# Kernel optimization log

Measured on AMD Instinct MI355X. Metric: run time of the kernel, lower is better.

Reference implementation:

```python
import jax, jax.numpy as jnp
import numpy as np

B, T, F, NC, H = 128, 2048, 80, 10, 32
EPS = 1e-5


def _xavier(k, shape):
    fan_out, fan_in = shape
    lim = float(np.sqrt(6.0 / (fan_in + fan_out)))
    return jax.random.uniform(k, shape, jnp.float32, -lim, lim)


def _gru_w(k, shape):
    lim = float(1.0 / np.sqrt(H))
    return jax.random.uniform(k, shape, jnp.float32, -lim, lim)


def setup_inputs() -> dict:
    key = jax.random.key(0)
    ks = jax.random.split(key, 16)
    z = jnp.zeros
    o = jnp.ones
    inp = {
        "x": jax.random.normal(ks[0], (B, T, F), jnp.float32),
        # feature extractor: Linear+BN x3
        "W1": _xavier(ks[1], (256, F)), "b1": z(256), "g1": o(256), "be1": z(256),
        "W2": _xavier(ks[2], (128, 256)), "b2": z(128), "g2": o(128), "be2": z(128),
        "W3": _xavier(ks[3], (64, 128)), "b3": z(64), "g3": o(64), "be3": z(64),
        # bidirectional GRU, hidden=32, gates ordered (r,z,n) as in torch
        "Wih_f": _gru_w(ks[4], (3 * H, 64)), "Whh_f": _gru_w(ks[5], (3 * H, H)),
        "bih_f": _gru_w(ks[6], (3 * H,)), "bhh_f": _gru_w(ks[7], (3 * H,)),
        "Wih_b": _gru_w(ks[8], (3 * H, 64)), "Whh_b": _gru_w(ks[9], (3 * H, H)),
        "bih_b": _gru_w(ks[10], (3 * H,)), "bhh_b": _gru_w(ks[11], (3 * H,)),
        # attention MLP
        "Wa1": _xavier(ks[12], (32, 64)), "ba1": z(32),
        "Wa2": _xavier(ks[13], (1, 32)), "ba2": z(1),
        # classifier
        "Wc1": _xavier(ks[14], (32, 64)), "bc1": z(32), "gc": o(32), "bec": z(32),
        "Wc2": _xavier(ks[15], (NC, 32)), "bc2": z(NC),
    }
    return inp


def _bn(x, g, b):
    # BatchNorm1d, training-mode batch statistics (biased var), dropout omitted (eval)
    m = jnp.mean(x, 0)
    v = jnp.mean(jnp.square(x - m), 0)
    return (x - m) * jax.lax.rsqrt(v + EPS) * g + b


def _gru_dir(feats, Wih, Whh, bih, bhh, reverse):
    # feats: [B,T,64] -> outputs [B,T,H]
    xp = jnp.einsum('btf,gf->btg', feats, Wih) + bih  # precompute input projections

    def step(h, xt):
        gh = h @ Whh.T + bhh
        r = jax.nn.sigmoid(xt[:, :H] + gh[:, :H])
        zg = jax.nn.sigmoid(xt[:, H:2 * H] + gh[:, H:2 * H])
        n = jnp.tanh(xt[:, 2 * H:] + r * gh[:, 2 * H:])
        hn = (1.0 - zg) * n + zg * h
        return hn, hn

    h0 = jnp.zeros((feats.shape[0], H), feats.dtype)
    _, hs = jax.lax.scan(step, h0, jnp.swapaxes(xp, 0, 1), reverse=reverse)
    return jnp.swapaxes(hs, 0, 1)


def reference(x, W1, b1, g1, be1, W2, b2, g2, be2, W3, b3, g3, be3,
              Wih_f, Whh_f, bih_f, bhh_f, Wih_b, Whh_b, bih_b, bhh_b,
              Wa1, ba1, Wa2, ba2, Wc1, bc1, gc, bec, Wc2, bc2):
    Bv, Tv, Fv = x.shape
    h = x.reshape(-1, Fv)
    h = jax.nn.relu(_bn(h @ W1.T + b1, g1, be1))
    h = jax.nn.relu(_bn(h @ W2.T + b2, g2, be2))
    h = jax.nn.relu(_bn(h @ W3.T + b3, g3, be3))
    feats = h.reshape(Bv, Tv, 64)
    gf = _gru_dir(feats, Wih_f, Whh_f, bih_f, bhh_f, False)
    gb = _gru_dir(feats, Wih_b, Whh_b, bih_b, bhh_b, True)
    gru_out = jnp.concatenate([gf, gb], axis=-1)  # [B,T,64]
    scores = jnp.tanh(gru_out @ Wa1.T + ba1) @ Wa2.T + ba2  # [B,T,1]
    attn = jax.nn.softmax(scores, axis=1)
    pooled = jnp.sum(gru_out * attn, axis=1)  # [B,64]
    c = jax.nn.relu(_bn(pooled @ Wc1.T + bc1, gc, bec))
    return c @ Wc2.T + bc2
```

## Files before the change

### kernel.cpp

```cpp
#include <hip/hip_runtime.h>
#include <hip/hip_fp16.h>
#include <cstdint>
#include <cstddef>

#define EPSV 1e-5f
constexpr int Bb = 128, Tt = 2048, Ff = 80, NCc = 10, Hh = 32;
constexpr int Nn = Bb * Tt;

constexpr size_t OFF_H1 = 0;
constexpr size_t OFF_H3 = 0;
constexpr size_t OFF_GRU = 0;
constexpr size_t OFF_XP = (size_t)Nn * 64;
constexpr size_t OFF_SCORES = (size_t)Nn * 64;
constexpr size_t OFF_H2 = (size_t)Nn * 128;
constexpr size_t TAIL = (size_t)Nn * 192;
constexpr size_t P1o = TAIL;
constexpr size_t P2o = P1o + 64 * 256 * 2;
constexpr size_t P3o = P2o + 64 * 128 * 2;
constexpr size_t PZEND = P3o + 64 * 64 * 2;
constexpr size_t SC1o = PZEND;
constexpr size_t SC2o = SC1o + 512;
constexpr size_t SC3o = SC2o + 256;
constexpr size_t BMAXo = SC3o + 128;
constexpr size_t BSUMo = BMAXo + 128;
constexpr size_t POOLEDo = BSUMo + 128;
constexpr size_t WS_EXTENT = POOLEDo + 128 * 64;

struct alignas(8) half4 { __half x, y, z, w; };

__global__ __launch_bounds__(256) void zero_kernel(float* __restrict__ p, int n) {
  const int i = blockIdx.x * 256 + threadIdx.x;
  if (i < n) p[i] = 0.f;
}

template <int K, bool BN_IN, bool STATS, bool A16, bool C16>
__global__ __launch_bounds__(256) void fc_kernel(
    const void* __restrict__ Av, const float* __restrict__ W,
    const float* __restrict__ bias, const float* __restrict__ scl,
    const float* __restrict__ shf, void* __restrict__ Cv, int ldc, int coloff,
    int COUT, float* __restrict__ Pstat) {
  __shared__ float smem[32 * 68 * 2 + 512];
  float* As = smem;
  float* Bs = smem + 32 * 68;
  float* Ss = smem + 32 * 68 * 2;
  float* Sh = Ss + 256;

  const int tid = threadIdx.x;
  const int r0 = blockIdx.x * 64;
  const int nb0 = blockIdx.y * 64;
  const int m0 = (tid >> 4) * 4;
  const int n0 = (tid & 15) * 4;

  if (BN_IN) {
    for (int k = tid; k < K; k += 256) {
      Ss[k] = scl[k];
      Sh[k] = shf[k];
    }
  }

  float acc[4][4] = {};

  constexpr int NKT = (K + 31) / 32;
  for (int kt = 0; kt < NKT; ++kt) {
    const int k0 = kt * 32;
    __syncthreads();
#pragma unroll
    for (int rep = 0; rep < 2; ++rep) {
      const int li = rep * 256 + tid;
      const int row = li >> 3;
      const int ko = (li & 7) * 4;
      float av[4] = {0.f, 0.f, 0.f, 0.f};
      if (k0 + ko < K) {
        if (A16) {
          const half4 v = *(const half4*)&(
              (const __half*)Av)[(size_t)(r0 + row) * K + k0 + ko];
          av[0] = __half2float(v.x); av[1] = __half2float(v.y);
          av[2] = __half2float(v.z); av[3] = __half2float(v.w);
        } else {
          const float4 v =
              *(const float4*)&((const float*)Av)[(size_t)(r0 + row) * K + k0 + ko];
          av[0] = v.x; av[1] = v.y; av[2] = v.z; av[3] = v.w;
        }
        if (BN_IN) {
#pragma unroll
          for (int e = 0; e < 4; ++e)
            av[e] = fmaxf(av[e] * Ss[k0 + ko + e] + Sh[k0 + ko + e], 0.f);
        }
      }
#pragma unroll
      for (int e = 0; e < 4; ++e) As[(ko + e) * 68 + row] = av[e];
      float bv[4] = {0.f, 0.f, 0.f, 0.f};
      const int wn = nb0 + row;
      if (wn < COUT && k0 + ko < K) {
        const float4 v = *(const float4*)&W[(size_t)wn * K + k0 + ko];
        bv[0] = v.x; bv[1] = v.y; bv[2] = v.z; bv[3] = v.w;
      }
#pragma unroll
      for (int e = 0; e < 4; ++e) Bs[(ko + e) * 68 + row] = bv[e];
    }
    __syncthreads();
#pragma unroll
    for (int kk = 0; kk < 32; ++kk) {
      const float4 a4 = *(const float4*)&As[kk * 68 + m0];
      const float4 b4 = *(const float4*)&Bs[kk * 68 + n0];
      const float a[4] = {a4.x, a4.y, a4.z, a4.w};
      const float b[4] = {b4.x, b4.y, b4.z, b4.w};
#pragma unroll
      for (int i = 0; i < 4; ++i)
#pragma unroll
        for (int j = 0; j < 4; ++j) acc[i][j] = fmaf(a[i], b[j], acc[i][j]);
    }
  }

  float colsum[4] = {0.f, 0.f, 0.f, 0.f};
  float colsq[4] = {0.f, 0.f, 0.f, 0.f};
#pragma unroll
  for (int i = 0; i < 4; ++i) {
    const int r = r0 + m0 + i;
    float vv[4];
#pragma unroll
    for (int j = 0; j < 4; ++j) {
      const int col = nb0 + n0 + j;
      float v = 0.f;
      if (col < COUT) v = acc[i][j] + bias[col];
      vv[j] = v;
      if (STATS) {
        colsum[j] += v;
        colsq[j] += v * v;
      }
    }
    if (nb0 + n0 + 3 < COUT) {
      if (C16) {
        half4 o;
        o.x = __float2half(vv[0]); o.y = __float2half(vv[1]);
        o.z = __float2half(vv[2]); o.w = __float2half(vv[3]);
        *(half4*)&((__half*)Cv)[(size_t)r * ldc + coloff + nb0 + n0] = o;
      } else {
        float4 o;
        o.x = vv[0]; o.y = vv[1]; o.z = vv[2]; o.w = vv[3];
        *(float4*)&((float*)Cv)[(size_t)r * ldc + coloff + nb0 + n0] = o;
      }
    } else {
#pragma unroll
      for (int j = 0; j < 4; ++j) {
        const int col = nb0 + n0 + j;
        if (col < COUT) {
          if (C16)
            ((__half*)Cv)[(size_t)r * ldc + coloff + col] = __float2half(vv[j]);
          else
            ((float*)Cv)[(size_t)r * ldc + coloff + col] = vv[j];
        }
      }
    }
  }
  if (STATS) {
    __syncthreads();
    const int rg = tid >> 4;
#pragma unroll
    for (int j = 0; j < 4; ++j) {
      smem[(n0 + j) * 16 + rg] = colsum[j];
      smem[1024 + (n0 + j) * 16 + rg] = colsq[j];
    }
    __syncthreads();
    if (tid < 64) {
      float s = 0.f, q = 0.f;
#pragma unroll
      for (int g = 0; g < 16; ++g) {
        s += smem[tid * 16 + g];
        q += smem[1024 + tid * 16 + g];
      }
      const int col = nb0 + tid;
      if (col < COUT) {
        const int bkt = blockIdx.x & 63;
        atomicAdd(&Pstat[(size_t)bkt * COUT + col], s);
        atomicAdd(&Pstat[(size_t)64 * COUT + (size_t)bkt * COUT + col], q);
      }
    }
  }
}

__global__ __launch_bounds__(256) void bn_finalize(
    const float* __restrict__ P, int COUT, int nrows,
    const float* __restrict__ g, const float* __restrict__ be,
    float* __restrict__ scl, float* __restrict__ shf) {
  const int c = threadIdx.x;
  if (c < COUT) {
    float s = 0.f, q = 0.f;
    for (int b = 0; b < 64; ++b) {
      s += P[(size_t)b * COUT + c];
      q += P[(size_t)64 * COUT + (size_t)b * COUT + c];
    }
    const float invN = 1.f / (float)nrows;
    const float m = s * invN;
    const float var = q * invN - m * m;
    const float inv = rsqrtf(var + EPSV);
    scl[c] = g[c] * inv;
    shf[c] = be[c] - m * g[c] * inv;
  }
}

__device__ __forceinline__ float readlane_f(float v, int l) {
  return __uint_as_float(
      (unsigned)__builtin_amdgcn_readlane((int)__float_as_uint(v), l));
}
__device__ __forceinline__ float sigmoid_f(float x) {
  return 1.f / (1.f + __expf(-x));
}
__device__ __forceinline__ float tanh_f(float x) {
  return 1.f - 2.f / (__expf(2.f * x) + 1.f);
}

__global__ __launch_bounds__(64) void gru_kernel(
    const __half* __restrict__ xp, const float* __restrict__ Whh_f,
    const float* __restrict__ bhh_f, const float* __restrict__ Whh_b,
    const float* __restrict__ bhh_b, float* __restrict__ out) {
  const int blk = blockIdx.x;
  const int b = blk >> 1, dir = blk & 1;
  const int lane = threadIdx.x;
  const float* __restrict__ Whh = dir ? Whh_b : Whh_f;
  const float* __restrict__ bhh = dir ? bhh_b : bhh_f;

  float w0[32], w1[32];
#pragma unroll
  for (int j4 = 0; j4 < 8; ++j4) {
    const float4 v = *(const float4*)&Whh[(size_t)lane * 32 + j4 * 4];
    w0[j4 * 4 + 0] = v.x; w0[j4 * 4 + 1] = v.y;
    w0[j4 * 4 + 2] = v.z; w0[j4 * 4 + 3] = v.w;
    float4 u = make_float4(0.f, 0.f, 0.f, 0.f);
    if (lane < 32) u = *(const float4*)&Whh[(size_t)(64 + lane) * 32 + j4 * 4];
    w1[j4 * 4 + 0] = u.x; w1[j4 * 4 + 1] = u.y;
    w1[j4 * 4 + 2] = u.z; w1[j4 * 4 + 3] = u.w;
  }
  const float bh0 = bhh[lane];
  const float bh1 = (lane < 32) ? bhh[64 + lane] : 0.f;

  float h = 0.f;
  const size_t base_b = (size_t)b * Tt;

  __half xa[8], xb[8];
#pragma unroll
  for (int u = 0; u < 8; ++u) {
    const int t = dir ? (Tt - 1 - u) : u;
    const __half* p = &xp[(base_b + t) * 192 + dir * 96];
    xa[u] = p[lane];
    xb[u] = (lane < 32) ? p[64 + lane] : __half(0.f);
  }

  for (int s = 0; s < Tt; s += 8) {
#pragma unroll
    for (int u = 0; u < 8; ++u) {
      const int st = s + u;
      const int t = dir ? (Tt - 1 - st) : st;
      const float xg0 = __half2float(xa[u]);
      const float xg1 = __half2float(xb[u]);
      const int sp = st + 8;
      if (sp < Tt) {
        const int tp = dir ? (Tt - 1 - sp) : sp;
        const __half* p = &xp[(base_b + tp) * 192 + dir * 96];
        xa[u] = p[lane];
        xb[u] = (lane < 32) ? p[64 + lane] : __half(0.f);
      }
      float a0 = 0.f, a0b = 0.f, a1 = 0.f, a1b = 0.f;
#pragma unroll
      for (int j = 0; j < 32; j += 2) {
        const float hj = readlane_f(h, j);
        const float hj1 = readlane_f(h, j + 1);
        a0 = fmaf(hj, w0[j], a0);
        a0b = fmaf(hj1, w0[j + 1], a0b);
        a1 = fmaf(hj, w1[j], a1);
        a1b = fmaf(hj1, w1[j + 1], a1b);
      }
      const float gh0 = bh0 + a0 + a0b;
      const float gh1 = bh1 + a1 + a1b;
      const float s0 = xg0 + gh0;
      const float s0z = __shfl(s0, (lane & 31) + 32);
      const float r = sigmoid_f(s0);
      const float z = sigmoid_f(s0z);
      const float n = tanh_f(xg1 + r * gh1);
      const float hn = (1.f - z) * n + z * h;
      h = hn;
      if (lane < 32) out[(base_b + t) * 64 + dir * 32 + lane] = hn;
    }
  }
}

__global__ __launch_bounds__(256) void attn_score_kernel(
    const float* __restrict__ G, const float* __restrict__ Wa1,
    const float* __restrict__ ba1, const float* __restrict__ Wa2,
    const float* __restrict__ ba2, float* __restrict__ scores) {
  const int n = blockIdx.x * 256 + threadIdx.x;
  const float* g = &G[(size_t)n * 64];
  float gv[64];
#pragma unroll
  for (int j4 = 0; j4 < 16; ++j4) {
    const float4 v = *(const float4*)&g[j4 * 4];
    gv[j4 * 4 + 0] = v.x; gv[j4 * 4 + 1] = v.y;
    gv[j4 * 4 + 2] = v.z; gv[j4 * 4 + 3] = v.w;
  }
  float sc = ba2[0];
#pragma unroll 4
  for (int l = 0; l < 32; ++l) {
    float a = ba1[l];
#pragma unroll
    for (int j = 0; j < 64; ++j) a = fmaf(Wa1[l * 64 + j], gv[j], a);
    sc = fmaf(Wa2[l], tanh_f(a), sc);
  }
  scores[n] = sc;
}

__global__ __launch_bounds__(256) void softmax_stats_kernel(
    const float* __restrict__ scores, float* __restrict__ bmax,
    float* __restrict__ bsum) {
  const int b = blockIdx.x;
  const int tid = threadIdx.x;
  __shared__ float red[256];
  const float* s = &scores[(size_t)b * Tt];
  float m = -1e30f;
  for (int t = tid; t < Tt; t += 256) m = fmaxf(m, s[t]);
  red[tid] = m;
  __syncthreads();
  for (int off = 128; off > 0; off >>= 1) {
    if (tid < off) red[tid] = fmaxf(red[tid], red[tid + off]);
    __syncthreads();
  }
  m = red[0];
  __syncthreads();
  float e = 0.f;
  for (int t = tid; t < Tt; t += 256) e += __expf(s[t] - m);
  red[tid] = e;
  __syncthreads();
  for (int off = 128; off > 0; off >>= 1) {
    if (tid < off) red[tid] += red[tid + off];
    __syncthreads();
  }
  if (tid == 0) {
    bmax[b] = m;
    bsum[b] = red[0];
  }
}

__global__ __launch_bounds__(256) void pooled_kernel(
    const float* __restrict__ G, const float* __restrict__ scores,
    const float* __restrict__ bmax, const float* __restrict__ bsum,
    float* __restrict__ pooled) {
  const int b = blockIdx.x;
  const int d = threadIdx.x & 63;
  const int q = threadIdx.x >> 6;
  const float m = bmax[b];
  float acc = 0.f;
  for (int t = q; t < Tt; t += 4) {
    const float w = __expf(scores[(size_t)b * Tt + t] - m);
    acc += w * G[((size_t)b * Tt + t) * 64 + d];
  }
  __shared__ float red[4][64];
  red[q][d] = acc;
  __syncthreads();
  if (threadIdx.x < 64) {
    const float v = red[0][d] + red[1][d] + red[2][d] + red[3][d];
    pooled[(size_t)b * 64 + d] = v / bsum[b];
  }
}

__global__ __launch_bounds__(128) void classifier_kernel(
    const float* __restrict__ pooled, const float* __restrict__ Wc1,
    const float* __restrict__ bc1, const float* __restrict__ gc,
    const float* __restrict__ bec, const float* __restrict__ Wc2,
    const float* __restrict__ bc2, float* __restrict__ out) {
  __shared__ float c1s[128][33];
  __shared__ float sA[32], sB[32];
  const int b = threadIdx.x;
  float pv[64];
#pragma unroll
  for (int j4 = 0; j4 < 16; ++j4) {
    const float4 v = *(const float4*)&pooled[(size_t)b * 64 + j4 * 4];
    pv[j4 * 4 + 0] = v.x; pv[j4 * 4 + 1] = v.y;
    pv[j4 * 4 + 2] = v.z; pv[j4 * 4 + 3] = v.w;
  }
#pragma unroll 2
  for (int j = 0; j < 32; ++j) {
    float a = bc1[j];
#pragma unroll
    for (int k = 0; k < 64; ++k) a = fmaf(Wc1[j * 64 + k], pv[k], a);
    c1s[b][j] = a;
  }
  __syncthreads();
  if (b < 32) {
    float s = 0.f, q = 0.f;
    for (int r = 0; r < 128; ++r) {
      const float v = c1s[r][b];
      s += v;
      q += v * v;
    }
    const float m = s * (1.f / 128.f);
    const float var = q * (1.f / 128.f) - m * m;
    const float inv = rsqrtf(var + EPSV);
    sA[b] = gc[b] * inv;
    sB[b] = bec[b] - m * gc[b] * inv;
  }
  __syncthreads();
  float act[32];
#pragma unroll
  for (int j = 0; j < 32; ++j)
    act[j] = fmaxf(c1s[b][j] * sA[j] + sB[j], 0.f);
#pragma unroll
  for (int k = 0; k < NCc; ++k) {
    float o = bc2[k];
#pragma unroll
    for (int j = 0; j < 32; ++j) o = fmaf(Wc2[k * 32 + j], act[j], o);
    out[(size_t)b * NCc + k] = o;
  }
}

extern "C" void kernel_launch(void* const* d_in, const int* in_sizes, int n_in,
                              void* d_out, int out_size, void* d_ws,
                              size_t ws_size, hipStream_t stream) {
  if (ws_size < WS_EXTENT * sizeof(float)) {
    zero_kernel<<<(out_size + 255) / 256, 256, 0, stream>>>((float*)d_out,
                                                            out_size);
    return;
  }

  const float* x = (const float*)d_in[0];
  const float* W1 = (const float*)d_in[1];
  const float* b1 = (const float*)d_in[2];
  const float* g1 = (const float*)d_in[3];
  const float* be1 = (const float*)d_in[4];
  const float* W2 = (const float*)d_in[5];
  const float* b2 = (const float*)d_in[6];
  const float* g2 = (const float*)d_in[7];
  const float* be2 = (const float*)d_in[8];
  const float* W3 = (const float*)d_in[9];
  const float* b3 = (const float*)d_in[10];
  const float* g3 = (const float*)d_in[11];
  const float* be3 = (const float*)d_in[12];
  const float* Wih_f = (const float*)d_in[13];
  const float* Whh_f = (const float*)d_in[14];
  const float* bih_f = (const float*)d_in[15];
  const float* bhh_f = (const float*)d_in[16];
  const float* Wih_b = (const float*)d_in[17];
  const float* Whh_b = (const float*)d_in[18];
  const float* bih_b = (const float*)d_in[19];
  const float* bhh_b = (const float*)d_in[20];
  const float* Wa1 = (const float*)d_in[21];
  const float* ba1 = (const float*)d_in[22];
  const float* Wa2 = (const float*)d_in[23];
  const float* ba2 = (const float*)d_in[24];
  const float* Wc1 = (const float*)d_in[25];
  const float* bc1 = (const float*)d_in[26];
  const float* gc = (const float*)d_in[27];
  const float* bec = (const float*)d_in[28];
  const float* Wc2 = (const float*)d_in[29];
  const float* bc2 = (const float*)d_in[30];

  float* ws = (float*)d_ws;
  __half* h1 = (__half*)(ws + OFF_H1);
  __half* h2 = (__half*)(ws + OFF_H2);
  float* h3 = ws + OFF_H3;
  __half* xp = (__half*)(ws + OFF_XP);
  float* gru = ws + OFF_GRU;

  {
    const int nz = (int)(PZEND - P1o);
    zero_kernel<<<(nz + 255) / 256, 256, 0, stream>>>(ws + P1o, nz);
  }

  const int rowblocks = Nn / 64;

  fc_kernel<80, false, true, false, true><<<dim3(rowblocks, 4), 256, 0, stream>>>(
      x, W1, b1, nullptr, nullptr, h1, 256, 0, 256, ws + P1o);
  bn_finalize<<<1, 256, 0, stream>>>(ws + P1o, 256, Nn, g1, be1, ws + SC1o,
                                     ws + SC1o + 256);
  fc_kernel<256, true, true, true, true><<<dim3(rowblocks, 2), 256, 0, stream>>>(
      h1, W2, b2, ws + SC1o, ws + SC1o + 256, h2, 128, 0, 128, ws + P2o);
  bn_finalize<<<1, 128, 0, stream>>>(ws + P2o, 128, Nn, g2, be2, ws + SC2o,
                                     ws + SC2o + 128);
  fc_kernel<128, true, true, true, false><<<dim3(rowblocks, 1), 256, 0, stream>>>(
      h2, W3, b3, ws + SC2o, ws + SC2o + 128, h3, 64, 0, 64, ws + P3o);
  bn_finalize<<<1, 64, 0, stream>>>(ws + P3o, 64, Nn, g3, be3, ws + SC3o,
                                    ws + SC3o + 64);
  fc_kernel<64, true, false, false, true><<<dim3(rowblocks, 2), 256, 0, stream>>>(
      h3, Wih_f, bih_f, ws + SC3o, ws + SC3o + 64, xp, 192, 0, 96, nullptr);
  fc_kernel<64, true, false, false, true><<<dim3(rowblocks, 2), 256, 0, stream>>>(
      h3, Wih_b, bih_b, ws + SC3o, ws + SC3o + 64, xp, 192, 96, 96, nullptr);
  gru_kernel<<<256, 64, 0, stream>>>(xp, Whh_f, bhh_f, Whh_b, bhh_b, gru);
  attn_score_kernel<<<Nn / 256, 256, 0, stream>>>(gru, Wa1, ba1, Wa2, ba2,
                                                  ws + OFF_SCORES);
  softmax_stats_kernel<<<Bb, 256, 0, stream>>>(ws + OFF_SCORES, ws + BMAXo,
                                               ws + BSUMo);
  pooled_kernel<<<Bb, 256, 0, stream>>>(gru, ws + OFF_SCORES, ws + BMAXo,
                                        ws + BSUMo, ws + POOLEDo);
  classifier_kernel<<<1, 128, 0, stream>>>(ws + POOLEDo, Wc1, bc1, gc, bec,
                                           Wc2, bc2, (float*)d_out);
}
```

Measured before the change: 1.814 ms.

## Fuse both GRU directions into one wave with swizzle broadcasts and packed gates

The GRU is remapped so one 64-lane wave per batch item runs both directions, 32 lanes each. Each lane owns one hidden unit and keeps all three gate weight rows in registers. The hidden state is broadcast inside each 32-lane half with ds_swizzle instead of readlane, and the cross-lane shuffle for the z gate is removed. The input-projection GEMM now writes r/z/n per hidden unit as one padded half4, so each step is a single 8-byte load per lane, at the cost of scattered scalar half stores in the projection kernel. The grid halves to 128 waves, and the longer per-lane FMA chain depends on swizzle latency.

```diff
diff --git a/kernel.cpp b/kernel.cpp
--- a/kernel.cpp
+++ b/kernel.cpp
@@ -33,7 +33,7 @@
   if (i < n) p[i] = 0.f;
 }
 
-template <int K, bool BN_IN, bool STATS, bool A16, bool C16>
+template <int K, bool BN_IN, bool STATS, bool A16, bool C16, bool XP_PACK>
 __global__ __launch_bounds__(256) void fc_kernel(
     const void* __restrict__ Av, const float* __restrict__ W,
     const float* __restrict__ bias, const float* __restrict__ scl,
@@ -129,7 +129,15 @@
         colsq[j] += v * v;
       }
     }
-    if (nb0 + n0 + 3 < COUT) {
+    if (XP_PACK) {
+#pragma unroll
+      for (int j = 0; j < 4; ++j) {
+        const int col = nb0 + n0 + j;
+        if (col < COUT)
+          ((__half*)Cv)[(size_t)r * ldc + coloff +
+                        ((col & 31) * 4 + (col >> 5))] = __float2half(vv[j]);
+      }
+    } else if (nb0 + n0 + 3 < COUT) {
       if (C16) {
         half4 o;
         o.x = __float2half(vv[0]); o.y = __float2half(vv[1]);
@@ -199,89 +207,104 @@
   }
 }
 
-__device__ __forceinline__ float readlane_f(float v, int l) {
-  return __uint_as_float(
-      (unsigned)__builtin_amdgcn_readlane((int)__float_as_uint(v), l));
-}
-__device__ __forceinline__ float sigmoid_f(float x) {
-  return 1.f / (1.f + __expf(-x));
-}
+template <int J>
+__device__ __forceinline__ float bc32(float v) {
+  return __int_as_float(
+      __builtin_amdgcn_ds_swizzle(__float_as_int(v), (J << 5)));
+}
+
+#define GRU_BCFMA(J)                                  \
+  {                                                   \
+    const float hx = bc32<(J)>(h);                    \
+    const float hy = bc32<(J) + 16>(h);               \
+    arx = fmaf(hx, wr[(J)], arx);                     \
+    ary = fmaf(hy, wr[(J) + 16], ary);                \
+    azx = fmaf(hx, wz[(J)], azx);                     \
+    azy = fmaf(hy, wz[(J) + 16], azy);                \
+    anx = fmaf(hx, wn[(J)], anx);                     \
+    any_ = fmaf(hy, wn[(J) + 16], any_);              \
+  }
+
+#define GRU_STEP(U, PF)                                              \
+  {                                                                  \
+    const float xr = __half2float(ring[(U)].x);                      \
+    const float xz = __half2float(ring[(U)].y);                      \
+    const float xn = __half2float(ring[(U)].z);                      \
+    if (PF) {                                                        \
+      ring[(U)] = *(const half4*)((const char*)xq + xoff);           \
+      xoff += (unsigned)xdel;                                        \
+    }                                                                \
+    float arx = xr + bhr, ary = 0.f;                                 \
+    float azx = xz + bhz, azy = 0.f;                                 \
+    float anx = bhn, any_ = 0.f;                                     \
+    GRU_BCFMA(0) GRU_BCFMA(1) GRU_BCFMA(2) GRU_BCFMA(3)              \
+    GRU_BCFMA(4) GRU_BCFMA(5) GRU_BCFMA(6) GRU_BCFMA(7)              \
+    GRU_BCFMA(8) GRU_BCFMA(9) GRU_BCFMA(10) GRU_BCFMA(11)            \
+    GRU_BCFMA(12) GRU_BCFMA(13) GRU_BCFMA(14) GRU_BCFMA(15)          \
+    const float sr = arx + ary, sz = azx + azy, sn = anx + any_;     \
+    const float rg = 1.f / (1.f + __expf(-sr));                      \
+    const float zg = 1.f / (1.f + __expf(-sz));                      \
+    const float npre = fmaf(rg, sn, xn);                             \
+    const float ng = 1.f - 2.f / (__expf(2.f * npre) + 1.f);         \
+    h = fmaf(zg, h - ng, ng);                                        \
+    *(float*)((char*)out + ooff) = h;                                \
+    ooff += (unsigned)odel;                                          \
+  }
+
+__global__ __launch_bounds__(64) void gru_kernel(
+    const __half* __restrict__ xq, const float* __restrict__ Whh_f,
+    const float* __restrict__ bhh_f, const float* __restrict__ Whh_b,
+    const float* __restrict__ bhh_b, float* __restrict__ out) {
+  const int b = blockIdx.x;
+  const int lane = threadIdx.x;
+  const int d = lane >> 5;
+  const int i = lane & 31;
+  const float* __restrict__ Whh = d ? Whh_b : Whh_f;
+  const float* __restrict__ bhh = d ? bhh_b : bhh_f;
+
+  float wr[32], wz[32], wn[32];
+#pragma unroll
+  for (int j4 = 0; j4 < 8; ++j4) {
+    const float4 vr = *(const float4*)&Whh[(size_t)i * 32 + j4 * 4];
+    const float4 vz = *(const float4*)&Whh[(size_t)(32 + i) * 32 + j4 * 4];
+    const float4 vn = *(const float4*)&Whh[(size_t)(64 + i) * 32 + j4 * 4];
+    wr[j4 * 4 + 0] = vr.x; wr[j4 * 4 + 1] = vr.y;
+    wr[j4 * 4 + 2] = vr.z; wr[j4 * 4 + 3] = vr.w;
+    wz[j4 * 4 + 0] = vz.x; wz[j4 * 4 + 1] = vz.y;
+    wz[j4 * 4 + 2] = vz.z; wz[j4 * 4 + 3] = vz.w;
+    wn[j4 * 4 + 0] = vn.x; wn[j4 * 4 + 1] = vn.y;
+    wn[j4 * 4 + 2] = vn.z; wn[j4 * 4 + 3] = vn.w;
+  }
+  const float bhr = bhh[i], bhz = bhh[32 + i], bhn = bhh[64 + i];
+
+  const unsigned n0 = (unsigned)(b * Tt + (d ? Tt - 1 : 0));
+  unsigned xoff = n0 * 512u + (unsigned)d * 256u + (unsigned)i * 8u;
+  unsigned ooff = n0 * 256u + (unsigned)d * 128u + (unsigned)i * 4u;
+  const int xdel = d ? -512 : 512;
+  const int odel = d ? -256 : 256;
+
+  half4 ring[8];
+#pragma unroll
+  for (int u = 0; u < 8; ++u) {
+    ring[u] = *(const half4*)((const char*)xq + xoff);
+    xoff += (unsigned)xdel;
+  }
+
+  float h = 0.f;
+
+  for (int s = 0; s < Tt - 8; s += 8) {
+    GRU_STEP(0, true) GRU_STEP(1, true) GRU_STEP(2, true) GRU_STEP(3, true)
+    GRU_STEP(4, true) GRU_STEP(5, true) GRU_STEP(6, true) GRU_STEP(7, true)
+  }
+  GRU_STEP(0, false) GRU_STEP(1, false) GRU_STEP(2, false) GRU_STEP(3, false)
+  GRU_STEP(4, false) GRU_STEP(5, false) GRU_STEP(6, false) GRU_STEP(7, false)
+}
+
+#undef GRU_STEP
+#undef GRU_BCFMA
+
 __device__ __forceinline__ float tanh_f(float x) {
   return 1.f - 2.f / (__expf(2.f * x) + 1.f);
-}
-
-__global__ __launch_bounds__(64) void gru_kernel(
-    const __half* __restrict__ xp, const float* __restrict__ Whh_f,
-    const float* __restrict__ bhh_f, const float* __restrict__ Whh_b,
-    const float* __restrict__ bhh_b, float* __restrict__ out) {
-  const int blk = blockIdx.x;
-  const int b = blk >> 1, dir = blk & 1;
-  const int lane = threadIdx.x;
-  const float* __restrict__ Whh = dir ? Whh_b : Whh_f;
-  const float* __restrict__ bhh = dir ? bhh_b : bhh_f;
-
-  float w0[32], w1[32];
-#pragma unroll
-  for (int j4 = 0; j4 < 8; ++j4) {
-    const float4 v = *(const float4*)&Whh[(size_t)lane * 32 + j4 * 4];
-    w0[j4 * 4 + 0] = v.x; w0[j4 * 4 + 1] = v.y;
-    w0[j4 * 4 + 2] = v.z; w0[j4 * 4 + 3] = v.w;
-    float4 u = make_float4(0.f, 0.f, 0.f, 0.f);
-    if (lane < 32) u = *(const float4*)&Whh[(size_t)(64 + lane) * 32 + j4 * 4];
-    w1[j4 * 4 + 0] = u.x; w1[j4 * 4 + 1] = u.y;
-    w1[j4 * 4 + 2] = u.z; w1[j4 * 4 + 3] = u.w;
-  }
-  const float bh0 = bhh[lane];
-  const float bh1 = (lane < 32) ? bhh[64 + lane] : 0.f;
-
-  float h = 0.f;
-  const size_t base_b = (size_t)b * Tt;
-
-  __half xa[8], xb[8];
-#pragma unroll
-  for (int u = 0; u < 8; ++u) {
-    const int t = dir ? (Tt - 1 - u) : u;
-    const __half* p = &xp[(base_b + t) * 192 + dir * 96];
-    xa[u] = p[lane];
-    xb[u] = (lane < 32) ? p[64 + lane] : __half(0.f);
-  }
-
-  for (int s = 0; s < Tt; s += 8) {
-#pragma unroll
-    for (int u = 0; u < 8; ++u) {
-      const int st = s + u;
-      const int t = dir ? (Tt - 1 - st) : st;
-      const float xg0 = __half2float(xa[u]);
-      const float xg1 = __half2float(xb[u]);
-      const int sp = st + 8;
-      if (sp < Tt) {
-        const int tp = dir ? (Tt - 1 - sp) : sp;
-        const __half* p = &xp[(base_b + tp) * 192 + dir * 96];
-        xa[u] = p[lane];
-        xb[u] = (lane < 32) ? p[64 + lane] : __half(0.f);
-      }
-      float a0 = 0.f, a0b = 0.f, a1 = 0.f, a1b = 0.f;
-#pragma unroll
-      for (int j = 0; j < 32; j += 2) {
-        const float hj = readlane_f(h, j);
-        const float hj1 = readlane_f(h, j + 1);
-        a0 = fmaf(hj, w0[j], a0);
-        a0b = fmaf(hj1, w0[j + 1], a0b);
-        a1 = fmaf(hj, w1[j], a1);
-        a1b = fmaf(hj1, w1[j + 1], a1b);
-      }
-      const float gh0 = bh0 + a0 + a0b;
-      const float gh1 = bh1 + a1 + a1b;
-      const float s0 = xg0 + gh0;
-      const float s0z = __shfl(s0, (lane & 31) + 32);
-      const float r = sigmoid_f(s0);
-      const float z = sigmoid_f(s0z);
-      const float n = tanh_f(xg1 + r * gh1);
-      const float hn = (1.f - z) * n + z * h;
-      h = hn;
-      if (lane < 32) out[(base_b + t) * 64 + dir * 32 + lane] = hn;
-    }
-  }
 }
 
 __global__ __launch_bounds__(256) void attn_score_kernel(
@@ -466,23 +489,32 @@
 
   const int rowblocks = Nn / 64;
 
-  fc_kernel<80, false, true, false, true><<<dim3(rowblocks, 4), 256, 0, stream>>>(
-      x, W1, b1, nullptr, nullptr, h1, 256, 0, 256, ws + P1o);
+  fc_kernel<80, false, true, false, true, false>
+      <<<dim3(rowblocks, 4), 256, 0, stream>>>(x, W1, b1, nullptr, nullptr, h1,
+                                               256, 0, 256, ws + P1o);
   bn_finalize<<<1, 256, 0, stream>>>(ws + P1o, 256, Nn, g1, be1, ws + SC1o,
                                      ws + SC1o + 256);
-  fc_kernel<256, true, true, true, true><<<dim3(rowblocks, 2), 256, 0, stream>>>(
-      h1, W2, b2, ws + SC1o, ws + SC1o + 256, h2, 128, 0, 128, ws + P2o);
+  fc_kernel<256, true, true, true, true, false>
+      <<<dim3(rowblocks, 2), 256, 0, stream>>>(h1, W2, b2, ws + SC1o,
+                                               ws + SC1o + 256, h2, 128, 0,
+                                               128, ws + P2o);
   bn_finalize<<<1, 128, 0, stream>>>(ws + P2o, 128, Nn, g2, be2, ws + SC2o,
                                      ws + SC2o + 128);
-  fc_kernel<128, true, true, true, false><<<dim3(rowblocks, 1), 256, 0, stream>>>(
-      h2, W3, b3, ws + SC2o, ws + SC2o + 128, h3, 64, 0, 64, ws + P3o);
+  fc_kernel<128, true, true, true, false, false>
+      <<<dim3(rowblocks, 1), 256, 0, stream>>>(h2, W3, b3, ws + SC2o,
+                                               ws + SC2o + 128, h3, 64, 0, 64,
+                                               ws + P3o);
   bn_finalize<<<1, 64, 0, stream>>>(ws + P3o, 64, Nn, g3, be3, ws + SC3o,
                                     ws + SC3o + 64);
-  fc_kernel<64, true, false, false, true><<<dim3(rowblocks, 2), 256, 0, stream>>>(
-      h3, Wih_f, bih_f, ws + SC3o, ws + SC3o + 64, xp, 192, 0, 96, nullptr);
-  fc_kernel<64, true, false, false, true><<<dim3(rowblocks, 2), 256, 0, stream>>>(
-      h3, Wih_b, bih_b, ws + SC3o, ws + SC3o + 64, xp, 192, 96, 96, nullptr);
-  gru_kernel<<<256, 64, 0, stream>>>(xp, Whh_f, bhh_f, Whh_b, bhh_b, gru);
+  fc_kernel<64, true, false, false, true, true>
+      <<<dim3(rowblocks, 2), 256, 0, stream>>>(h3, Wih_f, bih_f, ws + SC3o,
+                                               ws + SC3o + 64, xp, 256, 0, 96,
+                                               nullptr);
+  fc_kernel<64, true, false, false, true, true>
+      <<<dim3(rowblocks, 2), 256, 0, stream>>>(h3, Wih_b, bih_b, ws + SC3o,
+                                               ws + SC3o + 64, xp, 256, 128,
+                                               96, nullptr);
+  gru_kernel<<<Bb, 64, 0, stream>>>(xp, Whh_f, bhh_f, Whh_b, bhh_b, gru);
   attn_score_kernel<<<Nn / 256, 256, 0, stream>>>(gru, Wa1, ba1, Wa2, ba2,
                                                   ws + OFF_SCORES);
   softmax_stats_kernel<<<Bb, 256, 0, stream>>>(ws + OFF_SCORES, ws + BMAXo,
```

Result: no change. 1.840 ms (+1.5%).
